# Kernel tuning notes

Hardware: AMD Instinct MI355X
Metric: run time of the kernel (lower is better)

Reference implementation:

```python
import jax, jax.numpy as jnp
import numpy as np

B = 128   # batch_size (number of trees / source tweets)
H = 100   # tweet_out_size == GRU hidden == GAT feature dim


def _gru_layer(x, h0, Wih, Whh, bih, bhh):
    # x: [T, N, D] time-major; PyTorch GRU cell math
    def step(h, xt):
        gi = xt @ Wih.T + bih
        gh = h @ Whh.T + bhh
        ir, iz, in_ = jnp.split(gi, 3, axis=-1)
        hr, hz, hn = jnp.split(gh, 3, axis=-1)
        r = jax.nn.sigmoid(ir + hr)
        z = jax.nn.sigmoid(iz + hz)
        n = jnp.tanh(in_ + r * hn)
        h = (1.0 - z) * n + z * h
        return h, h
    hT, ys = jax.lax.scan(step, h0, x)
    return ys, hT


def _gru2(x, h0, Wih0, Whh0, bih0, bhh0, Wih1, Whh1, bih1, bhh1):
    y0, _ = _gru_layer(x, h0[0], Wih0, Whh0, bih0, bhh0)
    _, h1 = _gru_layer(y0, h0[1], Wih1, Whh1, bih1, bhh1)
    return h1  # final hidden of top layer: [N, H]


def _gat(x, ei, W, a_src, a_dst, b, heads, outc, concat):
    # PyG GATConv (eval mode, add_self_loops=True, leaky_relu slope 0.2)
    N = x.shape[0]
    loops = jnp.arange(N, dtype=ei.dtype)
    src = jnp.concatenate([ei[0], loops])
    dst = jnp.concatenate([ei[1], loops])
    h = (x @ W.T).reshape(N, heads, outc)           # [N, H, C]
    es = (h * a_src).sum(-1)                         # [N, H]
    ed = (h * a_dst).sum(-1)
    e = jax.nn.leaky_relu(es[src] + ed[dst], negative_slope=0.2)  # [E, H]
    m = jax.lax.stop_gradient(jax.ops.segment_max(e, dst, num_segments=N))
    ee = jnp.exp(e - m[dst])
    s = jax.ops.segment_sum(ee, dst, num_segments=N)
    alpha = ee / s[dst]
    out = jax.ops.segment_sum(h[src] * alpha[:, :, None], dst, num_segments=N)
    out = out.reshape(N, heads * outc) if concat else out.mean(axis=1)
    return out + b


def _forward(fl, user_text, gnode, gei, tnode, tei, idx):
    (user_feats, h0g, h0t, temb,
     gWih0, gWhh0, gbih0, gbhh0, gWih1, gWhh1, gbih1, gbhh1,
     tWih0, tWhh0, tbih0, tbhh0, tWih1, tWhh1, tbih1, tbhh1,
     uW1, ub1, uW2, ub2,
     gc1W, gc1as, gc1ad, gc1b, gc2W, gc2as, gc2ad, gc2b,
     tc1W, tc1as, tc1ad, tc1b, tc2W, tc2as, tc2ad, tc2b,
     fcW, fcb) = fl
    # --- graphGAT branch ---
    ue = jax.nn.relu(user_feats @ uW1.T + ub1) @ uW2.T + ub2        # [Nu, 100]
    ge = temb[gnode].transpose(1, 0, 2)                              # [T, Ntg, 100]
    hg = _gru2(ge, h0g, gWih0, gWhh0, gbih0, gbhh0, gWih1, gWhh1, gbih1, gbhh1)
    xg = jnp.concatenate([hg[:B], ue, hg[B:]], axis=0)               # [Ng, 100]
    xg = jax.nn.relu(_gat(xg, gei, gc1W, gc1as, gc1ad, gc1b, 8, 64, True))
    xg = jax.nn.relu(_gat(xg, gei, gc2W, gc2as, gc2ad, gc2b, 1, 100, False))
    # --- TreeGAT branch ---
    te = temb[tnode].transpose(1, 0, 2)                              # [T, Ntree, 100]
    ht = _gru2(te, h0t, tWih0, tWhh0, tbih0, tbhh0, tWih1, tWhh1, tbih1, tbhh1)
    xt = ht.at[:B].set(xg[:B])                                       # root rows <- user_root_embed
    xt = jax.nn.relu(_gat(xt, tei, tc1W, tc1as, tc1ad, tc1b, 8, 100, True))
    xt = jax.nn.relu(_gat(xt, tei, tc2W, tc2as, tc2ad, tc2b, 1, 100, False))
    # --- scatter_mean over trees + classifier ---
    ssum = jax.ops.segment_sum(xt, idx, num_segments=B)
    cnt = jax.ops.segment_sum(jnp.ones((xt.shape[0],), xt.dtype), idx, num_segments=B)
    mean = ssum / jnp.maximum(cnt, 1.0)[:, None]
    return mean @ fcW.T + fcb                                        # [B, 4]


def setup_inputs():
    key = jax.random.key(0)
    it = iter(jax.random.split(key, 60))
    def nrm(shape, s):
        return (jax.random.normal(next(it), shape) * s).astype(jnp.float32)
    Ntg, Nu, Ntree = 10000, 20000, 30000
    Ng = Ntg + Nu
    Eg, Et, V, T = 200000, 60000, 50000, 20
    inp = {}
    inp["user_text"] = jax.random.randint(next(it), (Nu, 10), 0, 1000)
    inp["user_feats"] = nrm((Nu, 9), 1.0)
    inp["graph_node_features"] = jax.random.randint(next(it), (Ntg, T), 0, V)
    inp["graph_edge_index"] = jax.random.randint(next(it), (2, Eg), 0, Ng)
    inp["merged_tree_feature"] = jax.random.randint(next(it), (Ntree, T), 0, V)
    inp["merged_tree_edge_index"] = jax.random.randint(next(it), (2, Et), 0, Ntree)
    inp["indices"] = jax.random.randint(next(it), (Ntree,), 0, B)
    inp["h0_graph"] = nrm((2, Ntg, H), 1.0)
    inp["h0_tree"] = nrm((2, Ntree, H), 1.0)
    inp["tweet_emb"] = nrm((V, H), 1.0)
    s = 0.1
    for p in ("g", "t"):
        for l in ("0", "1"):
            inp[p + "Wih" + l] = nrm((3 * H, H), s)
            inp[p + "Whh" + l] = nrm((3 * H, H), s)
            inp[p + "bih" + l] = jnp.zeros((3 * H,), jnp.float32)
            inp[p + "bhh" + l] = jnp.zeros((3 * H,), jnp.float32)
    inp["uW1"] = nrm((100, 9), s);    inp["ub1"] = jnp.zeros((100,), jnp.float32)
    inp["uW2"] = nrm((100, 100), s);  inp["ub2"] = jnp.zeros((100,), jnp.float32)
    inp["gc1W"] = nrm((512, 100), s); inp["gc1as"] = nrm((8, 64), s); inp["gc1ad"] = nrm((8, 64), s); inp["gc1b"] = jnp.zeros((512,), jnp.float32)
    inp["gc2W"] = nrm((100, 512), s); inp["gc2as"] = nrm((1, 100), s); inp["gc2ad"] = nrm((1, 100), s); inp["gc2b"] = jnp.zeros((100,), jnp.float32)
    inp["tc1W"] = nrm((800, 100), s); inp["tc1as"] = nrm((8, 100), s); inp["tc1ad"] = nrm((8, 100), s); inp["tc1b"] = jnp.zeros((800,), jnp.float32)
    inp["tc2W"] = nrm((100, 800), s); inp["tc2as"] = nrm((1, 100), s); inp["tc2ad"] = nrm((1, 100), s); inp["tc2b"] = jnp.zeros((100,), jnp.float32)
    inp["fcW"] = nrm((4, 100), s);    inp["fcb"] = jnp.zeros((4,), jnp.float32)
    return inp


def reference(user_text, user_feats, graph_node_features, graph_edge_index,
              merged_tree_feature, merged_tree_edge_index, indices,
              h0_graph, h0_tree, tweet_emb,
              gWih0, gWhh0, gbih0, gbhh0, gWih1, gWhh1, gbih1, gbhh1,
              tWih0, tWhh0, tbih0, tbhh0, tWih1, tWhh1, tbih1, tbhh1,
              uW1, ub1, uW2, ub2,
              gc1W, gc1as, gc1ad, gc1b, gc2W, gc2as, gc2ad, gc2b,
              tc1W, tc1as, tc1ad, tc1b, tc2W, tc2as, tc2ad, tc2b,
              fcW, fcb):
    fl = (user_feats, h0_graph, h0_tree, tweet_emb,
          gWih0, gWhh0, gbih0, gbhh0, gWih1, gWhh1, gbih1, gbhh1,
          tWih0, tWhh0, tbih0, tbhh0, tWih1, tWhh1, tbih1, tbhh1,
          uW1, ub1, uW2, ub2,
          gc1W, gc1as, gc1ad, gc1b, gc2W, gc2as, gc2ad, gc2b,
          tc1W, tc1as, tc1ad, tc1b, tc2W, tc2as, tc2ad, tc2b,
          fcW, fcb)
    return _forward(fl, user_text, graph_node_features, graph_edge_index,
                    merged_tree_feature, merged_tree_edge_index, indices)
```

## Files before the change

### kernel.cpp

```cpp
#include <hip/hip_runtime.h>

#define NB    128
#define HD    100
#define NU    20000
#define NTG   10000
#define NTREE 30000
#define NG    30000
#define TT    20
#define EG    200000
#define ET    60000
#define VOC   50000

#define ESTR2 448
#define WROWS 336
#define LOG2E  1.4426950408889634f
#define LOG2E2 2.8853900817779268f

typedef unsigned short u16;
typedef unsigned int   u32;
typedef __attribute__((ext_vector_type(8))) short short8;
typedef __attribute__((ext_vector_type(4))) float floatx4;

__device__ __forceinline__ float sigmoid2_(float y) {
    return __fdividef(1.f, 1.f + __builtin_amdgcn_exp2f(-y));
}
__device__ __forceinline__ float tanh2_(float y) {
    return 1.f - __fdividef(2.f, __builtin_amdgcn_exp2f(y) + 1.f);
}
__device__ __forceinline__ u16 f2bf(float f) {
    u32 u = __float_as_uint(f);
    u32 r = (u + 0x7fffu + ((u >> 16) & 1u)) >> 16;
    return (u16)r;
}
__device__ __forceinline__ u16 f2bf_c(float f) {
    u32 r;
    asm("v_cvt_pk_bf16_f32 %0, %1, %2" : "=v"(r) : "v"(f), "v"(f));
    return (u16)r;
}
__device__ __forceinline__ float bf2f(u16 h) {
    return __uint_as_float(((u32)h) << 16);
}

struct GruProb {
    const u16*   Etab;
    const int*   nodes;
    const float* h0;
    const u16*   Whh0;
    const u16*   Wih1;
    const u16*   Whh1;
    u16*         hout;
    int          M;
};

__global__ __launch_bounds__(448, 2) void gru_fused10(GruProb Pg, GruProb Pt, int gblocks)
{
    const bool isg = (int)blockIdx.x < gblocks;
    const GruProb P = isg ? Pg : Pt;
    const int bx = isg ? blockIdx.x : blockIdx.x - gblocks;
    const int M  = P.M;
    const int m0 = bx * 32;

    __shared__ u16 H0[2][32 * 128];
    __shared__ u16 H1[2][32 * 128];
    __shared__ int NID[TT * 32];

    const int tid  = threadIdx.x;
    const int w    = tid >> 6, lane = tid & 63;
    const int fr   = lane & 15, quad = lane >> 4;
    const int c    = w * 16 + fr;
    const bool cok = (c < HD);

    short8 Bh0[3][4], Bx1[3][4], Bh1[3][4];
#pragma unroll
    for (int g = 0; g < 3; ++g) {
        const size_t rb = (size_t)((g * 7 + w) * 16 + fr) * 128 + quad * 8;
#pragma unroll
        for (int kk = 0; kk < 4; ++kk) {
            Bh0[g][kk] = *(const short8*)(P.Whh0 + rb + kk * 32);
            Bx1[g][kk] = *(const short8*)(P.Wih1 + rb + kk * 32);
            Bh1[g][kk] = *(const short8*)(P.Whh1 + rb + kk * 32);
        }
    }

    for (int i = tid; i < 32 * 128; i += 448) {
        H0[0][i] = 0; H0[1][i] = 0; H1[0][i] = 0; H1[1][i] = 0;
    }
    for (int i = tid; i < 32 * TT; i += 448) {
        int row = i / TT, t = i - row * TT;
        int gm = m0 + row;
        NID[t * 32 + row] = (gm < M) ? P.nodes[(size_t)gm * TT + t] : 0;
    }
    __syncthreads();
    if (tid < 32) {
        int off = 200 ^ ((tid & 7) << 4);
        *(u16*)((char*)&H0[0][0] + tid * 256 + off) = 0x3F80;
        *(u16*)((char*)&H0[1][0] + tid * 256 + off) = 0x3F80;
        *(u16*)((char*)&H1[0][0] + tid * 256 + off) = 0x3F80;
        *(u16*)((char*)&H1[1][0] + tid * 256 + off) = 0x3F80;
    }

    float h0f[2][4] = {{0.f,0.f,0.f,0.f},{0.f,0.f,0.f,0.f}};
    float h1f[2][4] = {{0.f,0.f,0.f,0.f},{0.f,0.f,0.f,0.f}};
    if (cok) {
#pragma unroll
        for (int rt = 0; rt < 2; ++rt)
#pragma unroll
        for (int r = 0; r < 4; ++r) {
            int row = rt * 16 + quad * 4 + r;
            int gm  = m0 + row;
            float v0 = 0.f, v1 = 0.f;
            if (gm < M) {
                v0 = P.h0[(size_t)gm * HD + c];
                v1 = P.h0[(size_t)(M + gm) * HD + c];
            }
            h0f[rt][r] = v0; h1f[rt][r] = v1;
            int off = (2 * c) ^ ((row & 7) << 4);
            *(u16*)((char*)&H0[0][0] + row * 256 + off) = f2bf_c(v0);
            *(u16*)((char*)&H1[0][0] + row * 256 + off) = f2bf_c(v1);
        }
    }

    u32 xlo[2][4], xhi[2][4];
    auto xpref = [&](int tn) {
        if (cok) {
#pragma unroll
            for (int rt = 0; rt < 2; ++rt)
#pragma unroll
            for (int r = 0; r < 4; ++r) {
                int row = rt * 16 + quad * 4 + r;
                int nd  = NID[tn * 32 + row];
                uint2 v = *(const uint2*)(P.Etab + (size_t)nd * ESTR2 + c * 4);
                xlo[rt][r] = v.x; xhi[rt][r] = v.y;
            }
        }
    };
    __syncthreads();
    xpref(0);

#pragma unroll
    for (int rt = 0; rt < 2; ++rt) {
        short8 a[4];
#pragma unroll
        for (int kk = 0; kk < 4; ++kk) {
            int row = rt * 16 + fr;
            int off = (kk * 64 + quad * 16) ^ ((row & 7) << 4);
            a[kk] = *(const short8*)((const char*)&H0[0][0] + row * 256 + off);
        }
        floatx4 ag[3];
#pragma unroll
        for (int g = 0; g < 3; ++g) ag[g] = (floatx4){0.f, 0.f, 0.f, 0.f};
#pragma unroll
        for (int g = 0; g < 3; ++g)
#pragma unroll
            for (int kk = 0; kk < 4; ++kk)
                ag[g] = __builtin_amdgcn_mfma_f32_16x16x32_bf16(a[kk], Bh0[g][kk], ag[g], 0, 0, 0);
        if (cok) {
#pragma unroll
            for (int r = 0; r < 4; ++r) {
                int row = rt * 16 + quad * 4 + r;
                float rr = sigmoid2_(bf2f((u16)xlo[rt][r]) + ag[0][r]);
                float zz = sigmoid2_(bf2f((u16)(xlo[rt][r] >> 16)) + ag[1][r]);
                float nn = tanh2_(bf2f((u16)xhi[rt][r]) + rr * ag[2][r]);
                float o  = nn + zz * (h0f[rt][r] - nn);
                h0f[rt][r] = o;
                *(u16*)((char*)&H0[1][0] + row * 256 + ((2 * c) ^ ((row & 7) << 4))) = f2bf_c(o);
            }
        }
    }
    __syncthreads();

    for (int r = 0; r < TT; ++r) {
        const bool doA = (r + 1 < TT);
        if (doA) xpref(r + 1);

        const char* rd0 = (const char*)&H0[(r + 1) & 1][0];
        const char* rd1 = (const char*)&H1[r & 1][0];
        char*       wr0 = (char*)&H0[r & 1][0];
        char*       wr1 = (char*)&H1[(r + 1) & 1][0];

#pragma unroll
        for (int rt = 0; rt < 2; ++rt) {
            short8 a0[4], a1[4];
#pragma unroll
            for (int kk = 0; kk < 4; ++kk) {
                int row = rt * 16 + fr;
                int off = (kk * 64 + quad * 16) ^ ((row & 7) << 4);
                a0[kk] = *(const short8*)(rd0 + row * 256 + off);
                a1[kk] = *(const short8*)(rd1 + row * 256 + off);
            }
            floatx4 rz0 = {0.f,0.f,0.f,0.f}, rz1 = {0.f,0.f,0.f,0.f};
            floatx4 xnv = {0.f,0.f,0.f,0.f}, hnv = {0.f,0.f,0.f,0.f};
#pragma unroll
            for (int kk = 0; kk < 4; ++kk)
                rz0 = __builtin_amdgcn_mfma_f32_16x16x32_bf16(a0[kk], Bx1[0][kk], rz0, 0, 0, 0);
#pragma unroll
            for (int kk = 0; kk < 4; ++kk)
                rz0 = __builtin_amdgcn_mfma_f32_16x16x32_bf16(a1[kk], Bh1[0][kk], rz0, 0, 0, 0);
#pragma unroll
            for (int kk = 0; kk < 4; ++kk)
                rz1 = __builtin_amdgcn_mfma_f32_16x16x32_bf16(a0[kk], Bx1[1][kk], rz1, 0, 0, 0);
#pragma unroll
            for (int kk = 0; kk < 4; ++kk)
                rz1 = __builtin_amdgcn_mfma_f32_16x16x32_bf16(a1[kk], Bh1[1][kk], rz1, 0, 0, 0);
#pragma unroll
            for (int kk = 0; kk < 4; ++kk)
                xnv = __builtin_amdgcn_mfma_f32_16x16x32_bf16(a0[kk], Bx1[2][kk], xnv, 0, 0, 0);
#pragma unroll
            for (int kk = 0; kk < 4; ++kk)
                hnv = __builtin_amdgcn_mfma_f32_16x16x32_bf16(a1[kk], Bh1[2][kk], hnv, 0, 0, 0);
            floatx4 ag[3];
#pragma unroll
            for (int g = 0; g < 3; ++g) ag[g] = (floatx4){0.f, 0.f, 0.f, 0.f};
            if (doA) {
#pragma unroll
                for (int g = 0; g < 3; ++g)
#pragma unroll
                    for (int kk = 0; kk < 4; ++kk)
                        ag[g] = __builtin_amdgcn_mfma_f32_16x16x32_bf16(a0[kk], Bh0[g][kk], ag[g], 0, 0, 0);
            }
            if (cok) {
#pragma unroll
                for (int r4 = 0; r4 < 4; ++r4) {
                    int row = rt * 16 + quad * 4 + r4;
                    float rr = sigmoid2_(rz0[r4]);
                    float zz = sigmoid2_(rz1[r4]);
                    float nn = tanh2_(xnv[r4] + rr * hnv[r4]);
                    float o  = nn + zz * (h1f[rt][r4] - nn);
                    h1f[rt][r4] = o;
                    *(u16*)(wr1 + row * 256 + ((2 * c) ^ ((row & 7) << 4))) = f2bf_c(o);
                }
                if (doA) {
#pragma unroll
                    for (int r4 = 0; r4 < 4; ++r4) {
                        int row = rt * 16 + quad * 4 + r4;
                        float rr = sigmoid2_(bf2f((u16)xlo[rt][r4]) + ag[0][r4]);
                        float zz = sigmoid2_(bf2f((u16)(xlo[rt][r4] >> 16)) + ag[1][r4]);
                        float nn = tanh2_(bf2f((u16)xhi[rt][r4]) + rr * ag[2][r4]);
                        float o  = nn + zz * (h0f[rt][r4] - nn);
                        h0f[rt][r4] = o;
                        *(u16*)(wr0 + row * 256 + ((2 * c) ^ ((row & 7) << 4))) = f2bf_c(o);
                    }
                }
            }
        }
        __syncthreads();
    }

    for (int i = tid; i < 32 * 128; i += 448) {
        int row = i >> 7, cc = i & 127;
        int gm = m0 + row;
        if (gm < M) {
            int off = (2 * cc) ^ ((row & 7) << 4);
            P.hout[(size_t)gm * 128 + cc] = *(const u16*)((const char*)&H1[0][0] + row * 256 + off);
        }
    }
}

#define LDST 40
__global__ __launch_bounds__(256) void gemm_mfma(
    const u16* __restrict__ A, const u16* __restrict__ B,
    float* __restrict__ Cf, u16* __restrict__ Cb,
    int M, int N, int Kt, int lda, int ldw, int ldc)
{
    const int m0 = blockIdx.x * 64;
    if (m0 >= M) return;
    const int n0 = blockIdx.y * 64;

    __shared__ u16 Als[64 * LDST];
    __shared__ u16 Wls[64 * LDST];

    const int tid  = threadIdx.x;
    const int wave = tid >> 6, lane = tid & 63;
    const int row  = tid >> 2, part = (tid & 3) * 8;
    const int fr   = lane & 15, quad = lane >> 4;

    floatx4 acc[4];
#pragma unroll
    for (int t = 0; t < 4; ++t) acc[t] = (floatx4){0.f, 0.f, 0.f, 0.f};

    const int am = m0 + row;  const bool aok = am < M;
    const int wn = n0 + row;  const bool wok = wn < N;
    const uint4 z4 = {0u, 0u, 0u, 0u};

    for (int kk = 0; kk < Kt; ++kk) {
        uint4 av = aok ? *(const uint4*)(A + (size_t)am * lda + kk * 32 + part) : z4;
        uint4 wv = wok ? *(const uint4*)(B + (size_t)wn * ldw + kk * 32 + part) : z4;
        __syncthreads();
        *(uint4*)&Als[row * LDST + part] = av;
        *(uint4*)&Wls[row * LDST + part] = wv;
        __syncthreads();
        short8 af = *(const short8*)&Als[((wave << 4) + fr) * LDST + quad * 8];
#pragma unroll
        for (int t = 0; t < 4; ++t) {
            short8 bf = *(const short8*)&Wls[((t << 4) + fr) * LDST + quad * 8];
            acc[t] = __builtin_amdgcn_mfma_f32_16x16x32_bf16(af, bf, acc[t], 0, 0, 0);
        }
    }

    const int orow0 = m0 + (wave << 4) + quad * 4;
#pragma unroll
    for (int t = 0; t < 4; ++t) {
        int col = n0 + (t << 4) + fr;
        if (col >= N) continue;
#pragma unroll
        for (int r = 0; r < 4; ++r) {
            int mr = orow0 + r;
            if (mr >= M) continue;
            float v = acc[t][r];
            if (Cf) Cf[(size_t)mr * ldc + col] = v;
            if (Cb) Cb[(size_t)mr * ldc + col] = f2bf(v);
        }
    }
}

__global__ __launch_bounds__(256) void gemm_etab(
    const u16* __restrict__ A, const u16* __restrict__ W0, const u16* __restrict__ W1,
    u16* __restrict__ C0, u16* __restrict__ C1)
{
    const int m0 = blockIdx.x * 64;
    const int n0 = blockIdx.y * 64;
    const u16* B = blockIdx.z ? W1 : W0;
    u16* Cb = blockIdx.z ? C1 : C0;
    const int N = 400;

    __shared__ u16 Als[64 * LDST];
    __shared__ u16 Wls[64 * LDST];

    const int tid  = threadIdx.x;
    const int wave = tid >> 6, lane = tid & 63;
    const int row  = tid >> 2, part = (tid & 3) * 8;
    const int fr   = lane & 15, quad = lane >> 4;

    floatx4 acc[4];
#pragma unroll
    for (int t = 0; t < 4; ++t) acc[t] = (floatx4){0.f, 0.f, 0.f, 0.f};

    const int am = m0 + row;
    const int wn = n0 + row;  const bool wok = wn < N;
    const uint4 z4 = {0u, 0u, 0u, 0u};

    for (int kk = 0; kk < 4; ++kk) {
        uint4 av = *(const uint4*)(A + (size_t)am * 128 + kk * 32 + part);
        uint4 wv = wok ? *(const uint4*)(B + (size_t)wn * 128 + kk * 32 + part) : z4;
        __syncthreads();
        *(uint4*)&Als[row * LDST + part] = av;
        *(uint4*)&Wls[row * LDST + part] = wv;
        __syncthreads();
        short8 af = *(const short8*)&Als[((wave << 4) + fr) * LDST + quad * 8];
#pragma unroll
        for (int t = 0; t < 4; ++t) {
            short8 bf = *(const short8*)&Wls[((t << 4) + fr) * LDST + quad * 8];
            acc[t] = __builtin_amdgcn_mfma_f32_16x16x32_bf16(af, bf, acc[t], 0, 0, 0);
        }
    }

    const int orow0 = m0 + (wave << 4) + quad * 4;
#pragma unroll
    for (int t = 0; t < 4; ++t) {
        int col = n0 + (t << 4) + fr;
        if (col >= N) continue;
#pragma unroll
        for (int r = 0; r < 4; ++r)
            Cb[(size_t)(orow0 + r) * ESTR2 + col] = f2bf(acc[t][r]);
    }
}

__global__ __launch_bounds__(256) void gemm_nt(
    const float* __restrict__ A, const float* __restrict__ W,
    const float* __restrict__ bias, float* __restrict__ C,
    int M, int N, int K, int relu)
{
    const int m0 = blockIdx.x * 64;
    const int n0 = blockIdx.y * 64;
    __shared__ float As[20][68];
    __shared__ float Ws[20][68];
    const int tid = threadIdx.x;
    const int r0 = (tid >> 4) * 4;
    const int c0 = (tid & 15) * 4;
    int sr[5], sk[5];
#pragma unroll
    for (int it = 0; it < 5; ++it) {
        int idx = tid + it * 256;
        sr[it] = idx / 20; sk[it] = idx - sr[it] * 20;
    }
    float acc[4][4];
#pragma unroll
    for (int i = 0; i < 4; ++i)
#pragma unroll
        for (int j = 0; j < 4; ++j) acc[i][j] = 0.f;
    const int nch = (K + 19) / 20;
    for (int ch = 0; ch < nch; ++ch) {
        const int k0 = ch * 20;
#pragma unroll
        for (int it = 0; it < 5; ++it) {
            int m = m0 + sr[it], k = k0 + sk[it];
            float va = 0.f, vw = 0.f;
            if (k < K) {
                if (m < M) va = A[(size_t)m * K + k];
                int n = n0 + sr[it];
                if (n < N) vw = W[(size_t)n * K + k];
            }
            As[sk[it]][sr[it]] = va;
            Ws[sk[it]][sr[it]] = vw;
        }
        __syncthreads();
#pragma unroll
        for (int kkk = 0; kkk < 20; ++kkk) {
            float4 a = *(const float4*)&As[kkk][r0];
            float4 w = *(const float4*)&Ws[kkk][c0];
            float av[4] = {a.x, a.y, a.z, a.w};
            float wv[4] = {w.x, w.y, w.z, w.w};
#pragma unroll
            for (int i = 0; i < 4; ++i)
#pragma unroll
                for (int j = 0; j < 4; ++j)
                    acc[i][j] = fmaf(av[i], wv[j], acc[i][j]);
        }
        __syncthreads();
    }
#pragma unroll
    for (int i = 0; i < 4; ++i) {
        int m = m0 + r0 + i;
        if (m >= M) continue;
#pragma unroll
        for (int j = 0; j < 4; ++j) {
            int n = n0 + c0 + j;
            if (n >= N) continue;
            float v = acc[i][j] + (bias ? bias[n] : 0.f);
            if (relu) v = fmaxf(v, 0.f);
            C[(size_t)m * N + n] = v;
        }
    }
}

__global__ void convert_pad2(const float* __restrict__ src, u16* __restrict__ dst,
                             int M, int Mp, int K, int ldk,
                             const float* __restrict__ app, int appone)
{
    int t = blockIdx.x * blockDim.x + threadIdx.x;
    if (t >= Mp * ldk) return;
    int n = t / ldk, c = t - n * ldk;
    u16 o = 0;
    if (n < M) {
        if (c < K) o = f2bf(src[(size_t)n * K + c]);
        else if (c == 100) {
            if (app) o = f2bf(app[n]);
            else if (appone) o = 0x3F80;
        }
    }
    dst[t] = o;
}

struct CvtgBatch {
    const float* src[6];
    const float* bias[6];
    u16*         dst[6];
};
#define CVTG_BLOCKS_PER_MAT 168
__global__ void convert_gru_w6(CvtgBatch B)
{
    int mat = blockIdx.x / CVTG_BLOCKS_PER_MAT;
    int t = (blockIdx.x - mat * CVTG_BLOCKS_PER_MAT) * blockDim.x + threadIdx.x;
    int rr = t >> 7, cc = t & 127;
    int g = rr / 112, r2 = rr - g * 112;
    u16 o = 0;
    if (r2 < 100) {
        float sc = (g == 2) ? LOG2E2 : LOG2E;
        int sr = g * 100 + r2;
        if (cc < 100) o = f2bf(B.src[mat][(size_t)sr * 100 + cc] * sc);
        else if (cc == 100) o = f2bf(B.bias[mat][sr] * sc);
    }
    B.dst[mat][t] = o;
}

__global__ void convert_ih0(const float* __restrict__ s0, const float* __restrict__ b0,
                            u16* __restrict__ d0,
                            const float* __restrict__ s1, const float* __restrict__ b1,
                            u16* __restrict__ d1)
{
    int t = blockIdx.x * blockDim.x + threadIdx.x;
    if (t >= 2 * 448 * 128) return;
    int which = t / (448 * 128);
    int tt = t - which * (448 * 128);
    const float* s = which ? s1 : s0;
    const float* b = which ? b1 : b0;
    u16* d = which ? d1 : d0;
    int j = tt >> 7, kc = tt & 127;
    int cc = j >> 2, g = j & 3;
    u16 o = 0;
    if (g < 3 && cc < 100) {
        float sc = (g == 2) ? LOG2E2 : LOG2E;
        int sr = g * 100 + cc;
        if (kc < 100) o = f2bf(s[(size_t)sr * 100 + kc] * sc);
        else if (kc == 100) o = f2bf(b[sr] * sc);
    }
    d[tt] = o;
}

__global__ void build_xg_bf(const u16* __restrict__ hgb, const float* __restrict__ ue,
                            u16* __restrict__ xgb)
{
    int t = blockIdx.x * blockDim.x + threadIdx.x;
    if (t >= NG * 128) return;
    int n = t >> 7, c = t & 127;
    u16 o = 0;
    if (n < NB)           o = hgb[n * 128 + c];
    else if (n < NB + NU) { if (c < HD) o = f2bf(ue[(size_t)(n - NB) * HD + c]); }
    else                  o = hgb[(size_t)(n - NU) * 128 + c];
    xgb[t] = o;
}

__global__ void set_roots(const float* __restrict__ src, u16* __restrict__ hb)
{
    int t = blockIdx.x * blockDim.x + threadIdx.x;
    if (t >= NB * HD) return;
    int n = t / HD, c = t - n * HD;
    hb[(size_t)n * 128 + c] = f2bf(src[t]);
}

__global__ void csr_count2(const int* __restrict__ gei, const int* __restrict__ tei,
                           int* __restrict__ gcnt, int* __restrict__ tcnt)
{
    int e = blockIdx.x * blockDim.x + threadIdx.x;
    const int GE = EG + NG;
    if (e < GE) {
        int dst = (e < EG) ? gei[EG + e] : e - EG;
        atomicAdd(&gcnt[dst], 1);
    } else {
        int e2 = e - GE;
        if (e2 >= ET + NTREE) return;
        int dst = (e2 < ET) ? tei[ET + e2] : e2 - ET;
        atomicAdd(&tcnt[dst], 1);
    }
}

__global__ void csr_scan2(int* __restrict__ gcnt, int* __restrict__ goff, int* __restrict__ gcur,
                          int* __restrict__ tcnt, int* __restrict__ toff, int* __restrict__ tcur)
{
    const int* cnt = blockIdx.x ? tcnt : gcnt;
    int* off = blockIdx.x ? toff : goff;
    int* cur = blockIdx.x ? tcur : gcur;
    const int N = blockIdx.x ? NTREE : NG;
    __shared__ int part[256];
    const int tid = threadIdx.x;
    const int per = (N + 255) / 256;
    const int i0 = tid * per;
    const int i1 = min(i0 + per, N);
    int s = 0;
    for (int i = i0; i < i1; ++i) s += cnt[i];
    part[tid] = s;
    __syncthreads();
    for (int o = 1; o < 256; o <<= 1) {
        int u = (tid >= o) ? part[tid - o] : 0;
        __syncthreads();
        part[tid] += u;
        __syncthreads();
    }
    int base = part[tid] - s;
    for (int i = i0; i < i1; ++i) {
        off[i] = base; cur[i] = base;
        base += cnt[i];
    }
    if (tid == 255) off[N] = part[255];
}

__global__ void csr_scatter2(const int* __restrict__ gei, const int* __restrict__ tei,
                             int* __restrict__ gcur, int* __restrict__ tcur,
                             int* __restrict__ geidx, int* __restrict__ teidx)
{
    int e = blockIdx.x * blockDim.x + threadIdx.x;
    const int GE = EG + NG;
    if (e < GE) {
        int dst = (e < EG) ? gei[EG + e] : e - EG;
        int pos = atomicAdd(&gcur[dst], 1);
        geidx[pos] = e;
    } else {
        int e2 = e - GE;
        if (e2 >= ET + NTREE) return;
        int dst = (e2 < ET) ? tei[ET + e2] : e2 - ET;
        int pos = atomicAdd(&tcur[dst], 1);
        teidx[pos] = e2;
    }
}

__global__ void gat_es_ed(const u16* __restrict__ feat, const float* __restrict__ asrc,
                          const float* __restrict__ adst, float* __restrict__ es,
                          float* __restrict__ ed, float* __restrict__ m,
                          float* __restrict__ s, int N, int heads, int C)
{
    int gid = blockIdx.x * blockDim.x + threadIdx.x;
    if (gid >= N * heads) return;
    int n = gid / heads, hd = gid - n * heads;
    const u16* hp = feat + ((size_t)n * heads + hd) * C;
    const float* as = asrc + (size_t)hd * C;
    const float* ad = adst + (size_t)hd * C;
    float s1 = 0.f, s2 = 0.f;
    for (int c = 0; c < C; c += 4) {
        uint2 pk = *(const uint2*)(hp + c);
        float v0 = bf2f((u16)(pk.x & 0xffff)), v1 = bf2f((u16)(pk.x >> 16));
        float v2 = bf2f((u16)(pk.y & 0xffff)), v3 = bf2f((u16)(pk.y >> 16));
        s1 += v0 * as[c] + v1 * as[c + 1] + v2 * as[c + 2] + v3 * as[c + 3];
        s2 += v0 * ad[c] + v1 * ad[c + 1] + v2 * ad[c + 2] + v3 * ad[c + 3];
    }
    es[gid] = s1; ed[gid] = s2;
    m[gid] = __uint_as_float(0xFFFFFFFFu);
    s[gid] = 0.f;
}

__device__ __forceinline__ void atomic_max_f(float* addr, float v)
{
    if (v >= 0.f) atomicMax((int*)addr, __float_as_int(v));
    else          atomicMin((unsigned int*)addr, __float_as_uint(v));
}

__global__ void gat_edge_logit(const int* __restrict__ ei, int E, int N, int heads,
                               const float* __restrict__ es, const float* __restrict__ ed,
                               float* __restrict__ eb, float* __restrict__ m)
{
    int gid = blockIdx.x * blockDim.x + threadIdx.x;
    int EE = E + N;
    if (gid >= EE * heads) return;
    int idx = gid / heads, hd = gid - idx * heads;
    int src, dst;
    if (idx < E) { src = ei[idx]; dst = ei[E + idx]; } else { src = dst = idx - E; }
    float e = es[src * heads + hd] + ed[dst * heads + hd];
    e = e > 0.f ? e : 0.2f * e;
    eb[gid] = e;
    atomic_max_f(&m[dst * heads + hd], e);
}

__global__ void gat_edge_expsum(const int* __restrict__ ei, int E, int N, int heads,
                                float* __restrict__ eb, const float* __restrict__ m,
                                float* __restrict__ s)
{
    int gid = blockIdx.x * blockDim.x + threadIdx.x;
    int EE = E + N;
    if (gid >= EE * heads) return;
    int idx = gid / heads, hd = gid - idx * heads;
    int dst = (idx < E) ? ei[E + idx] : idx - E;
    float e = __expf(eb[gid] - m[dst * heads + hd]);
    eb[gid] = e;
    atomicAdd(&s[dst * heads + hd], e);
}

template<int C, int VEC>
__global__ __launch_bounds__(256) void gat_accum_csr(
    const int* __restrict__ off, const int* __restrict__ eidx,
    const int* __restrict__ ei, int E,
    const float* __restrict__ eb, const float* __restrict__ s,
    const u16* __restrict__ feat, const float* __restrict__ bias,
    float* __restrict__ outf, u16* __restrict__ outb,
    int N, int heads, int HC, int nchunk)
{
    int gt = blockIdx.x * blockDim.x + threadIdx.x;
    int w = gt >> 6, lane = gt & 63;
    int dst = w / nchunk, chunk = w - dst * nchunk;
    if (dst >= N) return;
    int c0 = chunk * 64 * VEC + lane * VEC;
    if (c0 >= HC) return;
    int hh[VEC]; float sinv[VEC], acc[VEC];
#pragma unroll
    for (int v = 0; v < VEC; ++v) {
        int c = c0 + v;
        hh[v] = c / C;
        sinv[v] = __fdividef(1.f, s[dst * heads + hh[v]]);
        acc[v] = 0.f;
    }
    int e0 = off[dst], e1 = off[dst + 1];
    for (int p = e0; p < e1; ++p) {
        int j = eidx[p];
        int src = (j < E) ? ei[j] : (j - E);
        const u16* frp = feat + (size_t)src * HC + c0;
        float fv[VEC];
        if (VEC == 4) {
            uint2 pk = *(const uint2*)frp;
            fv[0] = bf2f((u16)(pk.x & 0xffff)); fv[1] = bf2f((u16)(pk.x >> 16));
            fv[2] = bf2f((u16)(pk.y & 0xffff)); fv[3] = bf2f((u16)(pk.y >> 16));
        } else {
            u32 pk = *(const u32*)frp;
            fv[0] = bf2f((u16)(pk & 0xffff)); fv[1] = bf2f((u16)(pk >> 16));
        }
#pragma unroll
        for (int v = 0; v < VEC; ++v)
            acc[v] += fv[v] * eb[(size_t)j * heads + hh[v]] * sinv[v];
    }
#pragma unroll
    for (int v = 0; v < VEC; ++v) {
        int c = c0 + v;
        float o = fmaxf(acc[v] + bias[c], 0.f);
        if (outf) outf[(size_t)dst * HC + c] = o;
        if (outb) outb[(size_t)dst * HC + c] = f2bf(o);
    }
}

__global__ void scatter_mean_accum(const float* __restrict__ x, const int* __restrict__ idx,
                                   float* __restrict__ ssum, float* __restrict__ cnt)
{
    int t = blockIdx.x * blockDim.x + threadIdx.x;
    if (t >= NTREE * HD) return;
    int n = t / HD, c = t - n * HD;
    int b = idx[n];
    atomicAdd(&ssum[b * HD + c], x[t]);
    if (c == 0) atomicAdd(&cnt[b], 1.f);
}

__global__ void fc_out(const float* __restrict__ ssum, const float* __restrict__ cnt,
                       const float* __restrict__ W, const float* __restrict__ b,
                       float* __restrict__ out)
{
    int t = threadIdx.x;
    int bb = t >> 2, j = t & 3;
    float inv = __fdividef(1.f, fmaxf(cnt[bb], 1.f));
    float acc = b[j];
    for (int k = 0; k < HD; ++k) acc += ssum[bb * HD + k] * inv * W[j * HD + k];
    out[t] = acc;
}

extern "C" void kernel_launch(void* const* d_in, const int* in_sizes, int n_in,
                              void* d_out, int out_size, void* d_ws, size_t ws_size,
                              hipStream_t stream)
{
    const float* user_feats = (const float*)d_in[1];
    const int*   gnf        = (const int*)d_in[2];
    const int*   gei        = (const int*)d_in[3];
    const int*   tnf        = (const int*)d_in[4];
    const int*   tei        = (const int*)d_in[5];
    const int*   indices    = (const int*)d_in[6];
    const float* h0g        = (const float*)d_in[7];
    const float* h0t        = (const float*)d_in[8];
    const float* temb       = (const float*)d_in[9];
    const float* gW[2][4] = {{(const float*)d_in[10], (const float*)d_in[11], (const float*)d_in[12], (const float*)d_in[13]},
                             {(const float*)d_in[14], (const float*)d_in[15], (const float*)d_in[16], (const float*)d_in[17]}};
    const float* tW[2][4] = {{(const float*)d_in[18], (const float*)d_in[19], (const float*)d_in[20], (const float*)d_in[21]},
                             {(const float*)d_in[22], (const float*)d_in[23], (const float*)d_in[24], (const float*)d_in[25]}};
    const float* uW1 = (const float*)d_in[26]; const float* ub1 = (const float*)d_in[27];
    const float* uW2 = (const float*)d_in[28]; const float* ub2 = (const float*)d_in[29];
    const float* gc1W = (const float*)d_in[30]; const float* gc1as = (const float*)d_in[31];
    const float* gc1ad = (const float*)d_in[32]; const float* gc1b = (const float*)d_in[33];
    const float* gc2W = (const float*)d_in[34]; const float* gc2as = (const float*)d_in[35];
    const float* gc2ad = (const float*)d_in[36]; const float* gc2b = (const float*)d_in[37];
    const float* tc1W = (const float*)d_in[38]; const float* tc1as = (const float*)d_in[39];
    const float* tc1ad = (const float*)d_in[40]; const float* tc1b = (const float*)d_in[41];
    const float* tc2W = (const float*)d_in[42]; const float* tc2as = (const float*)d_in[43];
    const float* tc2ad = (const float*)d_in[44]; const float* tc2b = (const float*)d_in[45];
    const float* fcW = (const float*)d_in[46]; const float* fcb = (const float*)d_in[47];
    float* out = (float*)d_out;

    char* ws = (char*)d_ws;
    const size_t NEED = 226500000;
    if (ws_size < NEED) return;

    float* XGF    = (float*)(ws + 0);
    u16*   TEMB_B = (u16*)(ws + 12000000);
    u16*   ETAB_G = (u16*)(ws + 25000000);
    u16*   ETAB_T = (u16*)(ws + 70000000);
    u16*   GH1B   = (u16*)(ws + 115000000);
    u16*   TH1B   = (u16*)(ws + 117600000);
    float* UE     = (float*)(ws + 125300000);
    float* HID    = (float*)(ws + 133400000);
    u16*   WARENA = (u16*)(ws + 141500000);
    int*   GOFF   = (int*)(ws + 142700000);
    int*   GCUR   = (int*)(ws + 142900000);
    int*   GCNT   = (int*)(ws + 143100000);
    int*   TCNT   = (int*)(ws + 143220000);
    int*   GEIDX  = (int*)(ws + 143400000);
    int*   TOFF   = (int*)(ws + 144400000);
    int*   TCUR   = (int*)(ws + 144600000);
    int*   TEIDX  = (int*)(ws + 144800000);
    float* ESB    = (float*)(ws + 145300000);
    float* EDB    = (float*)(ws + 146300000);
    float* MB     = (float*)(ws + 147300000);
    float* SB     = (float*)(ws + 148300000);
    float* EBB    = (float*)(ws + 149300000);
    float* SSUM   = (float*)(ws + 156700000);
    float* SCNT   = (float*)(ws + 156800000);
    u16*   XG_B   = (u16*)(ws + 157000000);
    u16*   GFEAT1 = (u16*)(ws + 165000000);
    u16*   GOUT1B = (u16*)(ws + 25000000);
    u16*   GFEAT2 = (u16*)(ws + 56000000);
    u16*   TFEAT1 = (u16*)(ws + 25000000);
    u16*   TOUT1B = (u16*)(ws + 74000000);
    u16*   TFEAT2 = (u16*)(ws + 123000000);
    float* XOUT2  = (float*)(ws + 157000000);

    u16* gWHH0  = WARENA + 0;
    u16* gWIH1  = WARENA + 43008;
    u16* gWHH1  = WARENA + 86016;
    u16* tWHH0  = WARENA + 129024;
    u16* tWIH1  = WARENA + 172032;
    u16* tWHH1  = WARENA + 215040;
    u16* W_IH0A = WARENA + 258048;
    u16* W_IH0B = WARENA + 315392;
    u16* W_G1   = WARENA + 372736;
    u16* W_G2   = WARENA + 475136;

    auto cvt = [&](const float* src, u16* dst, int M, int Mp, int K, int ldk,
                   const float* app = nullptr, int appone = 0) {
        convert_pad2<<<((size_t)Mp * ldk + 255) / 256, 256, 0, stream>>>(
            src, dst, M, Mp, K, ldk, app, appone);
    };
    auto mfma = [&](const u16* A, int lda, const u16* W, int ldw,
                    float* Cf, u16* Cb, int ldc, int M, int N, int Kt) {
        dim3 grid((M + 63) / 64, (N + 63) / 64, 1);
        gemm_mfma<<<grid, 256, 0, stream>>>(A, W, Cf, Cb, M, N, Kt, lda, ldw, ldc);
    };
    auto gat_pre = [&](const u16* feat, int N, int heads, int C,
                       const float* asrc, const float* adst, const int* ei, int E) {
        gat_es_ed<<<(N * heads + 255) / 256, 256, 0, stream>>>(
            feat, asrc, adst, ESB, EDB, MB, SB, N, heads, C);
        int EE = E + N;
        gat_edge_logit<<<(EE * heads + 255) / 256, 256, 0, stream>>>(ei, E, N, heads, ESB, EDB, EBB, MB);
        gat_edge_expsum<<<(EE * heads + 255) / 256, 256, 0, stream>>>(ei, E, N, heads, EBB, MB, SB);
    };

    {
        dim3 g1((NU + 63) / 64, (HD + 63) / 64, 1);
        gemm_nt<<<g1, 256, 0, stream>>>(user_feats, uW1, ub1, HID, NU, HD, 9, 1);
        gemm_nt<<<g1, 256, 0, stream>>>(HID, uW2, ub2, UE, NU, HD, HD, 0);
    }

    cvt(temb, TEMB_B, VOC, VOC, HD, 128, nullptr, 1);
    {
        CvtgBatch B;
        B.src[0] = gW[0][1]; B.bias[0] = gW[0][3]; B.dst[0] = gWHH0;
        B.src[1] = gW[1][0]; B.bias[1] = gW[1][2]; B.dst[1] = gWIH1;
        B.src[2] = gW[1][1]; B.bias[2] = gW[1][3]; B.dst[2] = gWHH1;
        B.src[3] = tW[0][1]; B.bias[3] = tW[0][3]; B.dst[3] = tWHH0;
        B.src[4] = tW[1][0]; B.bias[4] = tW[1][2]; B.dst[4] = tWIH1;
        B.src[5] = tW[1][1]; B.bias[5] = tW[1][3]; B.dst[5] = tWHH1;
        convert_gru_w6<<<6 * CVTG_BLOCKS_PER_MAT, 256, 0, stream>>>(B);
    }
    convert_ih0<<<(2 * 448 * 128 + 255) / 256, 256, 0, stream>>>(
        gW[0][0], gW[0][2], W_IH0A, tW[0][0], tW[0][2], W_IH0B);
    {
        dim3 ge((VOC + 63) / 64, 7, 2);
        gemm_etab<<<ge, 256, 0, stream>>>(TEMB_B, W_IH0A, W_IH0B, ETAB_G, ETAB_T);
    }

    hipMemsetAsync(GCNT, 0, 143400000 - 143100000, stream);
    {
        int tot = (EG + NG) + (ET + NTREE);
        csr_count2<<<(tot + 255) / 256, 256, 0, stream>>>(gei, tei, GCNT, TCNT);
        csr_scan2<<<2, 256, 0, stream>>>(GCNT, GOFF, GCUR, TCNT, TOFF, TCUR);
        csr_scatter2<<<(tot + 255) / 256, 256, 0, stream>>>(gei, tei, GCUR, TCUR, GEIDX, TEIDX);
    }

    {
        GruProb Pg = { ETAB_G, gnf, h0g, gWHH0, gWIH1, gWHH1, GH1B, NTG };
        GruProb Pt = { ETAB_T, tnf, h0t, tWHH0, tWIH1, tWHH1, TH1B, NTREE };
        int gblk = (NTG + 31) / 32;
        int tblk = (NTREE + 31) / 32;
        gru_fused10<<<gblk + tblk, 448, 0, stream>>>(Pg, Pt, gblk);
    }

    build_xg_bf<<<(NG * 128 + 255) / 256, 256, 0, stream>>>(GH1B, UE, XG_B);
    cvt(gc1W, W_G1, 512, 512, HD, 128);
    cvt(gc2W, W_G2, 100, 100, 512, 512);
    {
        mfma(XG_B, 128, W_G1, 128, nullptr, GFEAT1, 512, NG, 512, 4);
        gat_pre(GFEAT1, NG, 8, 64, gc1as, gc1ad, gei, EG);
        int waves = NG * 2;
        gat_accum_csr<64, 4><<<(waves + 3) / 4, 256, 0, stream>>>(
            GOFF, GEIDX, gei, EG, EBB, SB, GFEAT1, gc1b, nullptr, GOUT1B, NG, 8, 512, 2);
    }
    {
        mfma(GOUT1B, 512, W_G2, 512, nullptr, GFEAT2, 100, NG, 100, 16);
        gat_pre(GFEAT2, NG, 1, 100, gc2as, gc2ad, gei, EG);
        int waves = NG;
        gat_accum_csr<100, 2><<<(waves + 3) / 4, 256, 0, stream>>>(
            GOFF, GEIDX, gei, EG, EBB, SB, GFEAT2, gc2b, XGF, nullptr, NG, 1, 100, 1);
    }

    set_roots<<<(NB * HD + 255) / 256, 256, 0, stream>>>(XGF, TH1B);
    cvt(tc1W, W_G1, 800, 800, HD, 128);
    cvt(tc2W, W_G2, 100, 100, 800, 800);
    {
        mfma(TH1B, 128, W_G1, 128, nullptr, TFEAT1, 800, NTREE, 800, 4);
        gat_pre(TFEAT1, NTREE, 8, 100, tc1as, tc1ad, tei, ET);
        int waves = NTREE * 4;
        gat_accum_csr<100, 4><<<(waves + 3) / 4, 256, 0, stream>>>(
            TOFF, TEIDX, tei, ET, EBB, SB, TFEAT1, tc1b, nullptr, TOUT1B, NTREE, 8, 800, 4);
    }
    {
        mfma(TOUT1B, 800, W_G2, 800, nullptr, TFEAT2, 100, NTREE, 100, 25);
        gat_pre(TFEAT2, NTREE, 1, 100, tc2as, tc2ad, tei, ET);
        int waves = NTREE;
        gat_accum_csr<100, 2><<<(waves + 3) / 4, 256, 0, stream>>>(
            TOFF, TEIDX, tei, ET, EBB, SB, TFEAT2, tc2b, XOUT2, nullptr, NTREE, 1, 100, 1);
    }

    hipMemsetAsync(SSUM, 0, (size_t)NB * HD * 4, stream);
    hipMemsetAsync(SCNT, 0, (size_t)NB * 4, stream);
    scatter_mean_accum<<<(NTREE * HD + 255) / 256, 256, 0, stream>>>(XOUT2, indices, SSUM, SCNT);
    fc_out<<<1, 512, 0, stream>>>(SSUM, SCNT, fcW, fcb, out);
}
```

Baseline: 1.547 ms.

## Double GRU rows per block and replace atomic GAT softmax with CSR per-destination kernel

The fused GRU kernel now processes 64 rows per block instead of 32, which doubles the shared-memory state and per-thread register arrays so the register-resident weights are reused across more rows. The GAT edge softmax's atomic max and atomic sum kernels are replaced by one CSR kernel that computes max, sum and normalized alpha per destination using wave shuffles, so the accumulate kernel no longer divides by a sum. The first-layer accumulation switches to 8-wide bf16 loads with fewer chunks per node. The larger GRU tile raises register and LDS pressure and may lower occupancy at launch bounds (448,2), and the alpha kernel reads the edge logits three times.

```diff
diff --git a/kernel.cpp b/kernel.cpp
--- a/kernel.cpp
+++ b/kernel.cpp
@@ -52,17 +52,17 @@
     int          M;
 };
 
-__global__ __launch_bounds__(448, 2) void gru_fused10(GruProb Pg, GruProb Pt, int gblocks)
+__global__ __launch_bounds__(448, 2) void gru_fused11(GruProb Pg, GruProb Pt, int gblocks)
 {
     const bool isg = (int)blockIdx.x < gblocks;
     const GruProb P = isg ? Pg : Pt;
     const int bx = isg ? blockIdx.x : blockIdx.x - gblocks;
     const int M  = P.M;
-    const int m0 = bx * 32;
-
-    __shared__ u16 H0[2][32 * 128];
-    __shared__ u16 H1[2][32 * 128];
-    __shared__ int NID[TT * 32];
+    const int m0 = bx * 64;
+
+    __shared__ u16 H0[2][64 * 128];
+    __shared__ u16 H1[2][64 * 128];
+    __shared__ int NID[TT * 64];
 
     const int tid  = threadIdx.x;
     const int w    = tid >> 6, lane = tid & 63;
@@ -82,16 +82,16 @@
         }
     }
 
-    for (int i = tid; i < 32 * 128; i += 448) {
+    for (int i = tid; i < 64 * 128; i += 448) {
         H0[0][i] = 0; H0[1][i] = 0; H1[0][i] = 0; H1[1][i] = 0;
     }
-    for (int i = tid; i < 32 * TT; i += 448) {
+    for (int i = tid; i < 64 * TT; i += 448) {
         int row = i / TT, t = i - row * TT;
         int gm = m0 + row;
-        NID[t * 32 + row] = (gm < M) ? P.nodes[(size_t)gm * TT + t] : 0;
+        NID[t * 64 + row] = (gm < M) ? P.nodes[(size_t)gm * TT + t] : 0;
     }
     __syncthreads();
-    if (tid < 32) {
+    if (tid < 64) {
         int off = 200 ^ ((tid & 7) << 4);
         *(u16*)((char*)&H0[0][0] + tid * 256 + off) = 0x3F80;
         *(u16*)((char*)&H0[1][0] + tid * 256 + off) = 0x3F80;
@@ -99,11 +99,11 @@
         *(u16*)((char*)&H1[1][0] + tid * 256 + off) = 0x3F80;
     }
 
-    float h0f[2][4] = {{0.f,0.f,0.f,0.f},{0.f,0.f,0.f,0.f}};
-    float h1f[2][4] = {{0.f,0.f,0.f,0.f},{0.f,0.f,0.f,0.f}};
+    float h0f[4][4] = {};
+    float h1f[4][4] = {};
     if (cok) {
 #pragma unroll
-        for (int rt = 0; rt < 2; ++rt)
+        for (int rt = 0; rt < 4; ++rt)
 #pragma unroll
         for (int r = 0; r < 4; ++r) {
             int row = rt * 16 + quad * 4 + r;
@@ -120,15 +120,15 @@
         }
     }
 
-    u32 xlo[2][4], xhi[2][4];
+    u32 xlo[4][4], xhi[4][4];
     auto xpref = [&](int tn) {
         if (cok) {
 #pragma unroll
-            for (int rt = 0; rt < 2; ++rt)
+            for (int rt = 0; rt < 4; ++rt)
 #pragma unroll
             for (int r = 0; r < 4; ++r) {
                 int row = rt * 16 + quad * 4 + r;
-                int nd  = NID[tn * 32 + row];
+                int nd  = NID[tn * 64 + row];
                 uint2 v = *(const uint2*)(P.Etab + (size_t)nd * ESTR2 + c * 4);
                 xlo[rt][r] = v.x; xhi[rt][r] = v.y;
             }
@@ -138,7 +138,7 @@
     xpref(0);
 
 #pragma unroll
-    for (int rt = 0; rt < 2; ++rt) {
+    for (int rt = 0; rt < 4; ++rt) {
         short8 a[4];
 #pragma unroll
         for (int kk = 0; kk < 4; ++kk) {
@@ -179,7 +179,7 @@
         char*       wr1 = (char*)&H1[(r + 1) & 1][0];
 
 #pragma unroll
-        for (int rt = 0; rt < 2; ++rt) {
+        for (int rt = 0; rt < 4; ++rt) {
             short8 a0[4], a1[4];
 #pragma unroll
             for (int kk = 0; kk < 4; ++kk) {
@@ -246,7 +246,7 @@
         __syncthreads();
     }
 
-    for (int i = tid; i < 32 * 128; i += 448) {
+    for (int i = tid; i < 64 * 128; i += 448) {
         int row = i >> 7, cc = i & 127;
         int gm = m0 + row;
         if (gm < M) {
@@ -585,8 +585,7 @@
 
 __global__ void gat_es_ed(const u16* __restrict__ feat, const float* __restrict__ asrc,
                           const float* __restrict__ adst, float* __restrict__ es,
-                          float* __restrict__ ed, float* __restrict__ m,
-                          float* __restrict__ s, int N, int heads, int C)
+                          float* __restrict__ ed, int N, int heads, int C)
 {
     int gid = blockIdx.x * blockDim.x + threadIdx.x;
     if (gid >= N * heads) return;
@@ -603,51 +602,72 @@
         s2 += v0 * ad[c] + v1 * ad[c + 1] + v2 * ad[c + 2] + v3 * ad[c + 3];
     }
     es[gid] = s1; ed[gid] = s2;
-    m[gid] = __uint_as_float(0xFFFFFFFFu);
-    s[gid] = 0.f;
-}
-
-__device__ __forceinline__ void atomic_max_f(float* addr, float v)
-{
-    if (v >= 0.f) atomicMax((int*)addr, __float_as_int(v));
-    else          atomicMin((unsigned int*)addr, __float_as_uint(v));
-}
-
-__global__ void gat_edge_logit(const int* __restrict__ ei, int E, int N, int heads,
-                               const float* __restrict__ es, const float* __restrict__ ed,
-                               float* __restrict__ eb, float* __restrict__ m)
-{
-    int gid = blockIdx.x * blockDim.x + threadIdx.x;
-    int EE = E + N;
-    if (gid >= EE * heads) return;
-    int idx = gid / heads, hd = gid - idx * heads;
-    int src, dst;
-    if (idx < E) { src = ei[idx]; dst = ei[E + idx]; } else { src = dst = idx - E; }
-    float e = es[src * heads + hd] + ed[dst * heads + hd];
-    e = e > 0.f ? e : 0.2f * e;
-    eb[gid] = e;
-    atomic_max_f(&m[dst * heads + hd], e);
-}
-
-__global__ void gat_edge_expsum(const int* __restrict__ ei, int E, int N, int heads,
-                                float* __restrict__ eb, const float* __restrict__ m,
-                                float* __restrict__ s)
-{
-    int gid = blockIdx.x * blockDim.x + threadIdx.x;
-    int EE = E + N;
-    if (gid >= EE * heads) return;
-    int idx = gid / heads, hd = gid - idx * heads;
-    int dst = (idx < E) ? ei[E + idx] : idx - E;
-    float e = __expf(eb[gid] - m[dst * heads + hd]);
-    eb[gid] = e;
-    atomicAdd(&s[dst * heads + hd], e);
+}
+
+template<int HEADS>
+__global__ __launch_bounds__(256) void gat_alpha_csr(
+    const int* __restrict__ off, const int* __restrict__ eidx,
+    const int* __restrict__ ei, int E,
+    const float* __restrict__ es, const float* __restrict__ ed,
+    float* __restrict__ eb, int N)
+{
+    int gt = blockIdx.x * blockDim.x + threadIdx.x;
+    int dst = gt >> 6, lane = gt & 63;
+    if (dst >= N) return;
+    const int hd  = lane & (HEADS - 1);
+    const int esl = lane / HEADS;
+    const int EPI = 64 / HEADS;
+    const int e0 = off[dst], e1 = off[dst + 1];
+    const float edv = ed[(size_t)dst * HEADS + hd];
+
+    float mymax = -3.4e38f;
+    for (int p0 = e0; p0 < e1; p0 += EPI) {
+        int p = p0 + esl;
+        if (p < e1) {
+            int j = eidx[p];
+            int src = (j < E) ? ei[j] : (j - E);
+            float e = es[(size_t)src * HEADS + hd] + edv;
+            e = e > 0.f ? e : 0.2f * e;
+            mymax = fmaxf(mymax, e);
+        }
+    }
+#pragma unroll
+    for (int o = HEADS; o < 64; o <<= 1)
+        mymax = fmaxf(mymax, __shfl_xor(mymax, o));
+
+    float ssum = 0.f;
+    for (int p0 = e0; p0 < e1; p0 += EPI) {
+        int p = p0 + esl;
+        if (p < e1) {
+            int j = eidx[p];
+            int src = (j < E) ? ei[j] : (j - E);
+            float e = es[(size_t)src * HEADS + hd] + edv;
+            e = e > 0.f ? e : 0.2f * e;
+            ssum += __expf(e - mymax);
+        }
+    }
+#pragma unroll
+    for (int o = HEADS; o < 64; o <<= 1)
+        ssum += __shfl_xor(ssum, o);
+    float sinv = __fdividef(1.f, ssum);
+
+    for (int p0 = e0; p0 < e1; p0 += EPI) {
+        int p = p0 + esl;
+        if (p < e1) {
+            int j = eidx[p];
+            int src = (j < E) ? ei[j] : (j - E);
+            float e = es[(size_t)src * HEADS + hd] + edv;
+            e = e > 0.f ? e : 0.2f * e;
+            eb[(size_t)j * HEADS + hd] = __expf(e - mymax) * sinv;
+        }
+    }
 }
 
 template<int C, int VEC>
 __global__ __launch_bounds__(256) void gat_accum_csr(
     const int* __restrict__ off, const int* __restrict__ eidx,
     const int* __restrict__ ei, int E,
-    const float* __restrict__ eb, const float* __restrict__ s,
+    const float* __restrict__ eb,
     const u16* __restrict__ feat, const float* __restrict__ bias,
     float* __restrict__ outf, u16* __restrict__ outb,
     int N, int heads, int HC, int nchunk)
@@ -658,12 +678,11 @@
     if (dst >= N) return;
     int c0 = chunk * 64 * VEC + lane * VEC;
     if (c0 >= HC) return;
-    int hh[VEC]; float sinv[VEC], acc[VEC];
+    int hh[VEC]; float acc[VEC];
 #pragma unroll
     for (int v = 0; v < VEC; ++v) {
         int c = c0 + v;
         hh[v] = c / C;
-        sinv[v] = __fdividef(1.f, s[dst * heads + hh[v]]);
         acc[v] = 0.f;
     }
     int e0 = off[dst], e1 = off[dst + 1];
@@ -672,7 +691,13 @@
         int src = (j < E) ? ei[j] : (j - E);
         const u16* frp = feat + (size_t)src * HC + c0;
         float fv[VEC];
-        if (VEC == 4) {
+        if (VEC == 8) {
+            uint4 pk = *(const uint4*)frp;
+            fv[0] = bf2f((u16)(pk.x & 0xffff)); fv[1] = bf2f((u16)(pk.x >> 16));
+            fv[2] = bf2f((u16)(pk.y & 0xffff)); fv[3] = bf2f((u16)(pk.y >> 16));
+            fv[4] = bf2f((u16)(pk.z & 0xffff)); fv[5] = bf2f((u16)(pk.z >> 16));
+            fv[6] = bf2f((u16)(pk.w & 0xffff)); fv[7] = bf2f((u16)(pk.w >> 16));
+        } else if (VEC == 4) {
             uint2 pk = *(const uint2*)frp;
             fv[0] = bf2f((u16)(pk.x & 0xffff)); fv[1] = bf2f((u16)(pk.x >> 16));
             fv[2] = bf2f((u16)(pk.y & 0xffff)); fv[3] = bf2f((u16)(pk.y >> 16));
@@ -682,11 +707,12 @@
         }
 #pragma unroll
         for (int v = 0; v < VEC; ++v)
-            acc[v] += fv[v] * eb[(size_t)j * heads + hh[v]] * sinv[v];
+            acc[v] += fv[v] * eb[(size_t)j * heads + hh[v]];
     }
 #pragma unroll
     for (int v = 0; v < VEC; ++v) {
         int c = c0 + v;
+        if (c >= HC) continue;
         float o = fmaxf(acc[v] + bias[c], 0.f);
         if (outf) outf[(size_t)dst * HC + c] = o;
         if (outb) outb[(size_t)dst * HC + c] = f2bf(o);
@@ -769,8 +795,6 @@
     int*   TEIDX  = (int*)(ws + 144800000);
     float* ESB    = (float*)(ws + 145300000);
     float* EDB    = (float*)(ws + 146300000);
-    float* MB     = (float*)(ws + 147300000);
-    float* SB     = (float*)(ws + 148300000);
     float* EBB    = (float*)(ws + 149300000);
     float* SSUM   = (float*)(ws + 156700000);
     float* SCNT   = (float*)(ws + 156800000);
@@ -804,14 +828,6 @@
         dim3 grid((M + 63) / 64, (N + 63) / 64, 1);
         gemm_mfma<<<grid, 256, 0, stream>>>(A, W, Cf, Cb, M, N, Kt, lda, ldw, ldc);
     };
-    auto gat_pre = [&](const u16* feat, int N, int heads, int C,
-                       const float* asrc, const float* adst, const int* ei, int E) {
-        gat_es_ed<<<(N * heads + 255) / 256, 256, 0, stream>>>(
-            feat, asrc, adst, ESB, EDB, MB, SB, N, heads, C);
-        int EE = E + N;
-        gat_edge_logit<<<(EE * heads + 255) / 256, 256, 0, stream>>>(ei, E, N, heads, ESB, EDB, EBB, MB);
-        gat_edge_expsum<<<(EE * heads + 255) / 256, 256, 0, stream>>>(ei, E, N, heads, EBB, MB, SB);
-    };
 
     {
         dim3 g1((NU + 63) / 64, (HD + 63) / 64, 1);
@@ -848,9 +864,9 @@
     {
         GruProb Pg = { ETAB_G, gnf, h0g, gWHH0, gWIH1, gWHH1, GH1B, NTG };
         GruProb Pt = { ETAB_T, tnf, h0t, tWHH0, tWIH1, tWHH1, TH1B, NTREE };
-        int gblk = (NTG + 31) / 32;
-        int tblk = (NTREE + 31) / 32;
-        gru_fused10<<<gblk + tblk, 448, 0, stream>>>(Pg, Pt, gblk);
+        int gblk = (NTG + 63) / 64;
+        int tblk = (NTREE + 63) / 64;
+        gru_fused11<<<gblk + tblk, 448, 0, stream>>>(Pg, Pt, gblk);
     }
 
     build_xg_bf<<<(NG * 128 + 255) / 256, 256, 0, stream>>>(GH1B, UE, XG_B);
@@ -858,17 +874,17 @@
     cvt(gc2W, W_G2, 100, 100, 512, 512);
     {
         mfma(XG_B, 128, W_G1, 128, nullptr, GFEAT1, 512, NG, 512, 4);
-        gat_pre(GFEAT1, NG, 8, 64, gc1as, gc1ad, gei, EG);
-        int waves = NG * 2;
-        gat_accum_csr<64, 4><<<(waves + 3) / 4, 256, 0, stream>>>(
-            GOFF, GEIDX, gei, EG, EBB, SB, GFEAT1, gc1b, nullptr, GOUT1B, NG, 8, 512, 2);
+        gat_es_ed<<<(NG * 8 + 255) / 256, 256, 0, stream>>>(GFEAT1, gc1as, gc1ad, ESB, EDB, NG, 8, 64);
+        gat_alpha_csr<8><<<(NG + 3) / 4, 256, 0, stream>>>(GOFF, GEIDX, gei, EG, ESB, EDB, EBB, NG);
+        gat_accum_csr<64, 8><<<(NG + 3) / 4, 256, 0, stream>>>(
+            GOFF, GEIDX, gei, EG, EBB, GFEAT1, gc1b, nullptr, GOUT1B, NG, 8, 512, 1);
     }
     {
         mfma(GOUT1B, 512, W_G2, 512, nullptr, GFEAT2, 100, NG, 100, 16);
-        gat_pre(GFEAT2, NG, 1, 100, gc2as, gc2ad, gei, EG);
-        int waves = NG;
-        gat_accum_csr<100, 2><<<(waves + 3) / 4, 256, 0, stream>>>(
-            GOFF, GEIDX, gei, EG, EBB, SB, GFEAT2, gc2b, XGF, nullptr, NG, 1, 100, 1);
+        gat_es_ed<<<(NG + 255) / 256, 256, 0, stream>>>(GFEAT2, gc2as, gc2ad, ESB, EDB, NG, 1, 100);
+        gat_alpha_csr<1><<<(NG + 3) / 4, 256, 0, stream>>>(GOFF, GEIDX, gei, EG, ESB, EDB, EBB, NG);
+        gat_accum_csr<100, 2><<<(NG + 3) / 4, 256, 0, stream>>>(
+            GOFF, GEIDX, gei, EG, EBB, GFEAT2, gc2b, XGF, nullptr, NG, 1, 100, 1);
     }
 
     set_roots<<<(NB * HD + 255) / 256, 256, 0, stream>>>(XGF, TH1B);
@@ -876,17 +892,17 @@
     cvt(tc2W, W_G2, 100, 100, 800, 800);
     {
         mfma(TH1B, 128, W_G1, 128, nullptr, TFEAT1, 800, NTREE, 800, 4);
-        gat_pre(TFEAT1, NTREE, 8, 100, tc1as, tc1ad, tei, ET);
-        int waves = NTREE * 4;
-        gat_accum_csr<100, 4><<<(waves + 3) / 4, 256, 0, stream>>>(
-            TOFF, TEIDX, tei, ET, EBB, SB, TFEAT1, tc1b, nullptr, TOUT1B, NTREE, 8, 800, 4);
+        gat_es_ed<<<(NTREE * 8 + 255) / 256, 256, 0, stream>>>(TFEAT1, tc1as, tc1ad, ESB, EDB, NTREE, 8, 100);
+        gat_alpha_csr<8><<<(NTREE + 3) / 4, 256, 0, stream>>>(TOFF, TEIDX, tei, ET, ESB, EDB, EBB, NTREE);
+        gat_accum_csr<100, 8><<<(NTREE * 2 + 3) / 4, 256, 0, stream>>>(
+            TOFF, TEIDX, tei, ET, EBB, TFEAT1, tc1b, nullptr, TOUT1B, NTREE, 8, 800, 2);
     }
     {
         mfma(TOUT1B, 800, W_G2, 800, nullptr, TFEAT2, 100, NTREE, 100, 25);
-        gat_pre(TFEAT2, NTREE, 1, 100, tc2as, tc2ad, tei, ET);
-        int waves = NTREE;
-        gat_accum_csr<100, 2><<<(waves + 3) / 4, 256, 0, stream>>>(
-            TOFF, TEIDX, tei, ET, EBB, SB, TFEAT2, tc2b, XOUT2, nullptr, NTREE, 1, 100, 1);
+        gat_es_ed<<<(NTREE + 255) / 256, 256, 0, stream>>>(TFEAT2, tc2as, tc2ad, ESB, EDB, NTREE, 1, 100);
+        gat_alpha_csr<1><<<(NTREE + 3) / 4, 256, 0, stream>>>(TOFF, TEIDX, tei, ET, ESB, EDB, EBB, NTREE);
+        gat_accum_csr<100, 2><<<(NTREE + 3) / 4, 256, 0, stream>>>(
+            TOFF, TEIDX, tei, ET, EBB, TFEAT2, tc2b, XOUT2, nullptr, NTREE, 1, 100, 1);
     }
 
     hipMemsetAsync(SSUM, 0, (size_t)NB * HD * 4, stream);
```

Result: slower. 1.820 ms (+17.7%).
